# Optimization experiments

Measured on AMD Instinct MI355X. Metric: run time of the kernel, lower is better.

The kernel has to match this reference:

```python
import jax, jax.numpy as jnp
import numpy as np

N_COUNTIES = 3144
P = 2
N_MOB = 6
N_COV = 10
T = 156
NNZ = 31440


def setup_inputs() -> dict:
    key = jax.random.key(0)
    ks = jax.random.split(key, 13)
    C = jax.random.uniform(ks[0], (T, N_COUNTIES), dtype=jnp.float32)
    D = jax.random.uniform(ks[1], (T, N_COUNTIES), dtype=jnp.float32)
    M = jax.random.uniform(ks[2], (N_MOB, T, N_COUNTIES), dtype=jnp.float32)
    cov = jax.random.normal(ks[3], (N_COV, N_COUNTIES), dtype=jnp.float32)
    B_nonzero = jax.random.normal(ks[4], (NNZ,), dtype=jnp.float32)
    A_nonzero = jax.random.normal(ks[5], (NNZ,), dtype=jnp.float32)
    H_nonzero = jax.random.normal(ks[6], (NNZ,), dtype=jnp.float32)
    mu = jax.random.normal(ks[7], (N_MOB, P), dtype=jnp.float32)
    nu = jax.random.normal(ks[8], (N_MOB, P), dtype=jnp.float32)
    upsilon = jax.random.normal(ks[9], (N_COV,), dtype=jnp.float32)
    zeta = jax.random.normal(ks[10], (N_COV,), dtype=jnp.float32)
    rows = jax.random.randint(ks[11], (NNZ,), 0, N_COUNTIES)
    cols = jax.random.randint(ks[12], (NNZ,), 0, N_COUNTIES)
    return dict(C=C, D=D, M=M, cov=cov, B_nonzero=B_nonzero, A_nonzero=A_nonzero,
                H_nonzero=H_nonzero, mu=mu, nu=nu, upsilon=upsilon, zeta=zeta,
                rows=rows, cols=cols)


def reference(C, D, M, cov, B_nonzero, A_nonzero, H_nonzero, mu, nu, upsilon, zeta, rows, cols):
    n = C.shape[1]
    p = mu.shape[1]
    Tp = C.shape[0] - p  # number of predicted steps (t = p .. T-1)

    # Dense scatter-built weight matrices (duplicates summed, matching
    # torch.sparse .to_dense()). The torch code reuses the SAME nonzero
    # vector for every lag tau, so B[tau] == B for all tau.
    B = jnp.zeros((n, n), C.dtype).at[rows, cols].add(B_nonzero)
    A = jnp.zeros((n, n), C.dtype).at[rows, cols].add(A_nonzero)
    H = jnp.zeros((n, n), C.dtype).at[rows, cols].add(H_nonzero)

    # Lagged windows: Cl[tau, i] = C[i + tau] == C[t - p + tau] for t = p + i.
    Cl = jnp.stack([C[tau:tau + Tp] for tau in range(p)], 0)  # [p, Tp, n]
    Dl = jnp.stack([D[tau:tau + Tp] for tau in range(p)], 0)  # [p, Tp, n]
    Ml = jnp.stack([M[:, tau:tau + Tp, :] for tau in range(p)], 1)  # [n_mob, p, Tp, n]

    # Since B[tau] are identical across lags, sum over p folds into one GEMM.
    c2c = jnp.einsum('ptn,nm->tm', Cl, B)  # [Tp, n]
    c2d = jnp.einsum('ptn,nm->tm', Cl, H)
    d2d = jnp.einsum('ptn,nm->tm', Dl, A)

    mob_c = jnp.einsum('kptn,kp->tn', Ml, mu)
    mob_d = jnp.einsum('kptn,kp->tn', Ml, nu)

    C_hat = c2c + mob_c + upsilon @ cov  # [Tp, n] (+ broadcast [n])
    D_hat = c2d + d2d + mob_d + zeta @ cov
    return C_hat, D_hat
```

## Files before the change

kernel.cpp:

```cpp
#include <hip/hip_runtime.h>


#define SCAN_TH 1024

__global__ void hist_and_transposeCD(const int* __restrict__ cols, int* __restrict__ counts,
                                     int NNZ,
                                     const float* __restrict__ C, const float* __restrict__ D,
                                     float* __restrict__ Ct, float* __restrict__ Dt,
                                     int T, int NC, int histBlocks, int cTiles, int tTiles) {
    if ((int)blockIdx.x < histBlocks) {
        int k = blockIdx.x * blockDim.x + threadIdx.x;
        if (k < NNZ) atomicAdd(&counts[cols[k]], 1);
        return;
    }
    __shared__ float tile[64][65];
    int bid = blockIdx.x - histBlocks;
    int z  = bid / (cTiles * tTiles);
    int r  = bid - z * cTiles * tTiles;
    int ct = r / tTiles;
    int tt = r - ct * tTiles;
    const float* src = z ? D : C;
    float* dst = z ? Dt : Ct;
    int lx = threadIdx.x & 63, ly = threadIdx.x >> 6;
    int c0 = ct * 64, t0 = tt * 64;
    for (int rr = ly; rr < 64; rr += 4) {
        int t = t0 + rr, c = c0 + lx;
        if (t < T && c < NC) tile[rr][lx] = src[(size_t)t * NC + c];
    }
    __syncthreads();
    for (int rr = ly; rr < 64; rr += 4) {
        int c = c0 + rr, t = t0 + lx;
        if (c < NC && t < T) dst[(size_t)c * T + t] = tile[lx][rr];
    }
}

__global__ __launch_bounds__(SCAN_TH)
void csr_scan(const int* __restrict__ counts, int* __restrict__ offsets,
              int* __restrict__ cursor, int NC) {
    __shared__ int ssum[SCAN_TH];
    int t = threadIdx.x;
    int chunk = (NC + SCAN_TH - 1) / SCAN_TH;
    int beg = t * chunk, end = min(beg + chunk, NC);
    int local = 0;
    for (int j = beg; j < end; ++j) local += counts[j];
    ssum[t] = local;
    __syncthreads();
    for (int off = 1; off < SCAN_TH; off <<= 1) {
        int v = (t >= off) ? ssum[t - off] : 0;
        __syncthreads();
        ssum[t] += v;
        __syncthreads();
    }
    int run = ssum[t] - local;
    for (int j = beg; j < end; ++j) {
        offsets[j] = run;
        cursor[j]  = run;
        run += counts[j];
    }
    if (t == SCAN_TH - 1) offsets[NC] = ssum[SCAN_TH - 1];
}

__global__ void csr_fill(const int* __restrict__ rows, const int* __restrict__ cols,
                         const float* __restrict__ Bnz, const float* __restrict__ Anz,
                         const float* __restrict__ Hnz,
                         int* __restrict__ cursor, float4* __restrict__ edges, int NNZ) {
    int k = blockIdx.x * blockDim.x + threadIdx.x;
    if (k >= NNZ) return;
    int s = cols[k];
    int pos = atomicAdd(&cursor[s], 1);
    edges[pos] = make_float4(__int_as_float(rows[k]), Bnz[k], Anz[k], Hnz[k]);
}

__global__ void sparse_wave(const float* __restrict__ Ct, const float* __restrict__ Dt,
                            const int* __restrict__ offsets, const float4* __restrict__ edges,
                            float* __restrict__ wsS0, float* __restrict__ wsS1,
                            int T, int TPn, int nChunks, int nWaves) {
    int gtid = blockIdx.x * blockDim.x + threadIdx.x;
    int wid = gtid >> 6, lane = threadIdx.x & 63;
    if (wid >= nWaves) return;
    int c = wid / nChunks;
    int chunk = wid - c * nChunks;
    int i = chunk * 64 + lane;
    bool valid = i < TPn;
    int isafe = valid ? i : 0;
    float a0 = 0.f, a1 = 0.f;
    int e0 = offsets[c], e1 = offsets[c + 1];
    for (int e = e0; e < e1; ++e) {
        float4 E = edges[e];
        int g = __float_as_int(E.x);
        const float* cr = Ct + (size_t)g * T;
        const float* dr = Dt + (size_t)g * T;
        float cs = cr[isafe] + cr[isafe + 1];
        float ds = dr[isafe] + dr[isafe + 1];
        a0 += cs * E.y;
        a1 += cs * E.w + ds * E.z;
    }
    if (valid) {
        wsS0[(size_t)c * TPn + i] = a0;
        wsS1[(size_t)c * TPn + i] = a1;
    }
}

#define FTI 32
#define FTC 32
__global__ void final_fuse(const float* __restrict__ wsS0, const float* __restrict__ wsS1,
                           const float* __restrict__ M,
                           const float* __restrict__ cov,
                           const float* __restrict__ mu,
                           const float* __restrict__ nu,
                           const float* __restrict__ ups, const float* __restrict__ zet,
                           float* __restrict__ out0, float* __restrict__ out1,
                           int T, int NC, int NMOB, int NCOV, int TPn, int cTiles) {
    __shared__ float s0[FTI][FTC + 1], s1[FTI][FTC + 1];
    int bi = blockIdx.x / cTiles;
    int bc = blockIdx.x - bi * cTiles;
    int i0 = bi * FTI, c0 = bc * FTC;
    int tid = threadIdx.x;

    {
        int li = tid & 31;
        int lc0 = tid >> 5;
        int i = i0 + li;
        for (int cc = lc0; cc < FTC; cc += 8) {
            int c = c0 + cc;
            float v0 = 0.f, v1 = 0.f;
            if (c < NC && i < TPn) {
                v0 = wsS0[(size_t)c * TPn + i];
                v1 = wsS1[(size_t)c * TPn + i];
            }
            s0[li][cc] = v0;
            s1[li][cc] = v1;
        }
    }
    __syncthreads();

    int lc = tid & 31;
    int ri = tid >> 5;
    int c = c0 + lc;
    if (c >= NC) return;

    float cv0 = 0.f, cv1 = 0.f;
    for (int j = 0; j < NCOV; ++j) {
        float cv = cov[(size_t)j * NC + c];
        cv0 += cv * ups[j];
        cv1 += cv * zet[j];
    }
    for (int ii = ri; ii < FTI; ii += 8) {
        int i = i0 + ii;
        if (i >= TPn) break;
        float a0 = s0[ii][lc] + cv0;
        float a1 = s1[ii][lc] + cv1;
        for (int k = 0; k < NMOB; ++k) {
            const float* mb = M + (size_t)k * T * NC;
            float m0 = mb[(size_t)i * NC + c];
            float m1 = mb[(size_t)(i + 1) * NC + c];
            a0 += m0 * mu[k * 2] + m1 * mu[k * 2 + 1];
            a1 += m0 * nu[k * 2] + m1 * nu[k * 2 + 1];
        }
        out0[(size_t)i * NC + c] = a0;
        out1[(size_t)i * NC + c] = a1;
    }
}

__global__ void fused_generic(const float* __restrict__ C, const float* __restrict__ D,
                              const float* __restrict__ M, const float* __restrict__ cov,
                              const float* __restrict__ mu, const float* __restrict__ nu,
                              const float* __restrict__ ups, const float* __restrict__ zet,
                              const int* __restrict__ offsets, const float4* __restrict__ edges,
                              float* __restrict__ out0, float* __restrict__ out1,
                              int T, int NC, int NMOB, int NCOV, int P, int TPn) {
    int idx = blockIdx.x * blockDim.x + threadIdx.x;
    if (idx >= TPn * NC) return;
    int i = idx / NC;
    int c = idx - i * NC;
    float acc0 = 0.f, acc1 = 0.f;
    for (int k = 0; k < NMOB; ++k)
        for (int tau = 0; tau < P; ++tau) {
            float m = M[((size_t)k * T + i + tau) * NC + c];
            acc0 += m * mu[k * P + tau];
            acc1 += m * nu[k * P + tau];
        }
    for (int j = 0; j < NCOV; ++j) {
        float cv = cov[(size_t)j * NC + c];
        acc0 += cv * ups[j];
        acc1 += cv * zet[j];
    }
    int e0 = offsets[c], e1 = offsets[c + 1];
    for (int e = e0; e < e1; ++e) {
        float4 E = edges[e];
        int g = __float_as_int(E.x);
        float cs = 0.f, ds = 0.f;
        for (int tau = 0; tau < P; ++tau) {
            cs += C[(size_t)(i + tau) * NC + g];
            ds += D[(size_t)(i + tau) * NC + g];
        }
        acc0 += cs * E.y;
        acc1 += cs * E.w + ds * E.z;
    }
    out0[idx] = acc0;
    out1[idx] = acc1;
}

extern "C" void kernel_launch(void* const* d_in, const int* in_sizes, int n_in,
                              void* d_out, int out_size, void* d_ws, size_t ws_size,
                              hipStream_t stream) {
    const float* C    = (const float*)d_in[0];
    const float* D    = (const float*)d_in[1];
    const float* M    = (const float*)d_in[2];
    const float* cov  = (const float*)d_in[3];
    const float* Bnz  = (const float*)d_in[4];
    const float* Anz  = (const float*)d_in[5];
    const float* Hnz  = (const float*)d_in[6];
    const float* mu   = (const float*)d_in[7];
    const float* nu   = (const float*)d_in[8];
    const float* ups  = (const float*)d_in[9];
    const float* zet  = (const float*)d_in[10];
    const int*  rows  = (const int*)d_in[11];
    const int*  cols  = (const int*)d_in[12];

    int NCOV = in_sizes[9];
    int NC   = in_sizes[3] / NCOV;
    int T    = in_sizes[0] / NC;
    int NMOB = in_sizes[2] / in_sizes[0];
    int P    = in_sizes[7] / NMOB;
    int NNZ  = in_sizes[11];
    int TPn  = T - P;

    float* out0 = (float*)d_out;
    float* out1 = out0 + (size_t)TPn * NC;

    float4* edges   = (float4*)d_ws;
    int*    offsets = (int*)(edges + NNZ);
    int*    counts  = offsets + (NC + 1);
    int*    cursor  = counts + NC;
    float*  Ct      = (float*)(cursor + NC);
    float*  Dt      = Ct + (size_t)NC * T;
    float*  wsS0    = Dt + (size_t)NC * T;
    float*  wsS1    = wsS0 + (size_t)NC * TPn;
    size_t  need    = (size_t)((char*)(wsS1 + (size_t)NC * TPn) - (char*)d_ws);

    const int BS = 256;
    hipMemsetAsync(counts, 0, (size_t)NC * sizeof(int), stream);

    if (P == 2 && ws_size >= need) {
        int histBlocks = (NNZ + BS - 1) / BS;
        int cT64 = (NC + 63) / 64, tT64 = (T + 63) / 64;
        hist_and_transposeCD<<<histBlocks + 2 * cT64 * tT64, BS, 0, stream>>>(
            cols, counts, NNZ, C, D, Ct, Dt, T, NC, histBlocks, cT64, tT64);

        csr_scan<<<1, SCAN_TH, 0, stream>>>(counts, offsets, cursor, NC);
        csr_fill<<<(NNZ + BS - 1) / BS, BS, 0, stream>>>(
            rows, cols, Bnz, Anz, Hnz, cursor, edges, NNZ);

        int nChunks = (TPn + 63) / 64;
        int nWaves  = NC * nChunks;
        sparse_wave<<<(nWaves * 64 + BS - 1) / BS, BS, 0, stream>>>(
            Ct, Dt, offsets, edges, wsS0, wsS1, T, TPn, nChunks, nWaves);

        int iTiles = (TPn + FTI - 1) / FTI;
        int cTiles = (NC + FTC - 1) / FTC;
        final_fuse<<<iTiles * cTiles, BS, 0, stream>>>(
            wsS0, wsS1, M, cov, mu, nu, ups, zet,
            out0, out1, T, NC, NMOB, NCOV, TPn, cTiles);
    } else {
        csr_hist_only:;
        hist_and_transposeCD<<<(NNZ + BS - 1) / BS, BS, 0, stream>>>(
            cols, counts, NNZ, C, D, (float*)d_ws, (float*)d_ws, T, NC,
            (NNZ + BS - 1) / BS, 0, 0);
        csr_scan<<<1, SCAN_TH, 0, stream>>>(counts, offsets, cursor, NC);
        csr_fill<<<(NNZ + BS - 1) / BS, BS, 0, stream>>>(
            rows, cols, Bnz, Anz, Hnz, cursor, edges, NNZ);
        int n = TPn * NC;
        fused_generic<<<(n + BS - 1) / BS, BS, 0, stream>>>(
            C, D, M, cov, mu, nu, ups, zet, offsets, edges,
            out0, out1, T, NC, NMOB, NCOV, P, TPn);
    }
}
```

Before: 141.8 us.

## Replace CSR build and two-stage sparse pass with per-tile edge filtering megakernel

```diff
diff --git a/kernel.cpp b/kernel.cpp
--- a/kernel.cpp
+++ b/kernel.cpp
@@ -1,24 +1,21 @@
 #include <hip/hip_runtime.h>
 
 
+#define BS     256
+#define CTILE  32
+#define ITILE  32
+#define ECAP   3072
 #define SCAN_TH 1024
 
-__global__ void hist_and_transposeCD(const int* __restrict__ cols, int* __restrict__ counts,
-                                     int NNZ,
-                                     const float* __restrict__ C, const float* __restrict__ D,
-                                     float* __restrict__ Ct, float* __restrict__ Dt,
-                                     int T, int NC, int histBlocks, int cTiles, int tTiles) {
-    if ((int)blockIdx.x < histBlocks) {
-        int k = blockIdx.x * blockDim.x + threadIdx.x;
-        if (k < NNZ) atomicAdd(&counts[cols[k]], 1);
-        return;
-    }
+__global__ void transposeCD(const float* __restrict__ C, const float* __restrict__ D,
+                            float* __restrict__ Ct, float* __restrict__ Dt,
+                            int T, int NC, int cT, int tT) {
     __shared__ float tile[64][65];
-    int bid = blockIdx.x - histBlocks;
-    int z  = bid / (cTiles * tTiles);
-    int r  = bid - z * cTiles * tTiles;
-    int ct = r / tTiles;
-    int tt = r - ct * tTiles;
+    int bid = blockIdx.x;
+    int z  = bid / (cT * tT);
+    int r  = bid - z * cT * tT;
+    int ct = r / tT;
+    int tt = r - ct * tT;
     const float* src = z ? D : C;
     float* dst = z ? Dt : Ct;
     int lx = threadIdx.x & 63, ly = threadIdx.x >> 6;
@@ -34,6 +31,127 @@
     }
 }
 
+__global__ __launch_bounds__(BS)
+void mega(const float* __restrict__ Ct,
+          const float* __restrict__ Dt,
+          const float* __restrict__ M,
+          const float* __restrict__ cov,
+          const float* __restrict__ mu,
+          const float* __restrict__ nu,
+          const float* __restrict__ ups,
+          const float* __restrict__ zet,
+          const int*  __restrict__ rows,
+          const int*  __restrict__ cols,
+          const float* __restrict__ Bnz,
+          const float* __restrict__ Anz,
+          const float* __restrict__ Hnz,
+          float* __restrict__ out0, float* __restrict__ out1,
+          int T, int NC, int NMOB, int NCOV, int NNZ, int TPn, int cTiles) {
+    __shared__ int   s_edge[ECAP];
+    __shared__ float s_a0[CTILE][ITILE + 1];
+    __shared__ float s_a1[CTILE][ITILE + 1];
+    __shared__ int   s_scan[BS];
+
+    int bi = blockIdx.x / cTiles;
+    int bc = blockIdx.x - bi * cTiles;
+    int i0 = bi * ITILE, c0 = bc * CTILE;
+    int tid = threadIdx.x;
+    int cmax = NC - c0; if (cmax > CTILE) cmax = CTILE;
+
+    for (int x = tid; x < CTILE * (ITILE + 1); x += BS) {
+        ((float*)s_a0)[x] = 0.f;
+        ((float*)s_a1)[x] = 0.f;
+    }
+
+    int cnt = 0;
+    for (int k = tid; k < NNZ; k += BS) {
+        int cl = cols[k] - c0;
+        if ((unsigned)cl < (unsigned)cmax) cnt++;
+    }
+    s_scan[tid] = cnt;
+    __syncthreads();
+    for (int off = 1; off < BS; off <<= 1) {
+        int v = (tid >= off) ? s_scan[tid - off] : 0;
+        __syncthreads();
+        s_scan[tid] += v;
+        __syncthreads();
+    }
+    int total = s_scan[BS - 1];
+    int wpos = s_scan[tid] - cnt;
+    if (total <= ECAP) {
+        for (int k = tid; k < NNZ; k += BS) {
+            int cl = cols[k] - c0;
+            if ((unsigned)cl < (unsigned)cmax) s_edge[wpos++] = (k << 5) | cl;
+        }
+    }
+    __syncthreads();
+
+    int li  = tid & 31;
+    int grp = tid >> 5;
+    int iA  = i0 + li;
+    int isafe = (iA < TPn) ? iA : (TPn - 1);
+    if (total <= ECAP) {
+        for (int e = grp; e < total; e += 8) {
+            int pk = s_edge[e];
+            int k = pk >> 5, cl = pk & 31;
+            int g = rows[k];
+            float Bv = Bnz[k], Av = Anz[k], Hv = Hnz[k];
+            const float* cr = Ct + (size_t)g * T;
+            const float* dr = Dt + (size_t)g * T;
+            float cs = cr[isafe] + cr[isafe + 1];
+            float ds = dr[isafe] + dr[isafe + 1];
+            atomicAdd(&s_a0[cl][li], cs * Bv);
+            atomicAdd(&s_a1[cl][li], cs * Hv + ds * Av);
+        }
+    } else {
+        for (int k = grp; k < NNZ; k += 8) {
+            int cl = cols[k] - c0;
+            if ((unsigned)cl < (unsigned)cmax) {
+                int g = rows[k];
+                float Bv = Bnz[k], Av = Anz[k], Hv = Hnz[k];
+                const float* cr = Ct + (size_t)g * T;
+                const float* dr = Dt + (size_t)g * T;
+                float cs = cr[isafe] + cr[isafe + 1];
+                float ds = dr[isafe] + dr[isafe + 1];
+                atomicAdd(&s_a0[cl][li], cs * Bv);
+                atomicAdd(&s_a1[cl][li], cs * Hv + ds * Av);
+            }
+        }
+    }
+    __syncthreads();
+
+    int lc = tid & 31;
+    int ri = tid >> 5;
+    int c = c0 + lc;
+    if (c >= NC) return;
+
+    float cv0 = 0.f, cv1 = 0.f;
+    for (int j = 0; j < NCOV; ++j) {
+        float cv = cov[(size_t)j * NC + c];
+        cv0 += cv * ups[j];
+        cv1 += cv * zet[j];
+    }
+    for (int ii = ri; ii < ITILE; ii += 8) {
+        int io = i0 + ii;
+        if (io >= TPn) break;
+        float a0 = s_a0[lc][ii] + cv0;
+        float a1 = s_a1[lc][ii] + cv1;
+        for (int k = 0; k < NMOB; ++k) {
+            const float* mb = M + (size_t)k * T * NC;
+            float m0 = mb[(size_t)io * NC + c];
+            float m1 = mb[(size_t)(io + 1) * NC + c];
+            a0 += m0 * mu[k * 2] + m1 * mu[k * 2 + 1];
+            a1 += m0 * nu[k * 2] + m1 * nu[k * 2 + 1];
+        }
+        out0[(size_t)io * NC + c] = a0;
+        out1[(size_t)io * NC + c] = a1;
+    }
+}
+
+__global__ void csr_hist(const int* __restrict__ cols, int* __restrict__ counts, int NNZ) {
+    int k = blockIdx.x * blockDim.x + threadIdx.x;
+    if (k < NNZ) atomicAdd(&counts[cols[k]], 1);
+}
 __global__ __launch_bounds__(SCAN_TH)
 void csr_scan(const int* __restrict__ counts, int* __restrict__ offsets,
               int* __restrict__ cursor, int NC) {
@@ -59,7 +177,6 @@
     }
     if (t == SCAN_TH - 1) offsets[NC] = ssum[SCAN_TH - 1];
 }
-
 __global__ void csr_fill(const int* __restrict__ rows, const int* __restrict__ cols,
                          const float* __restrict__ Bnz, const float* __restrict__ Anz,
                          const float* __restrict__ Hnz,
@@ -70,98 +187,6 @@
     int pos = atomicAdd(&cursor[s], 1);
     edges[pos] = make_float4(__int_as_float(rows[k]), Bnz[k], Anz[k], Hnz[k]);
 }
-
-__global__ void sparse_wave(const float* __restrict__ Ct, const float* __restrict__ Dt,
-                            const int* __restrict__ offsets, const float4* __restrict__ edges,
-                            float* __restrict__ wsS0, float* __restrict__ wsS1,
-                            int T, int TPn, int nChunks, int nWaves) {
-    int gtid = blockIdx.x * blockDim.x + threadIdx.x;
-    int wid = gtid >> 6, lane = threadIdx.x & 63;
-    if (wid >= nWaves) return;
-    int c = wid / nChunks;
-    int chunk = wid - c * nChunks;
-    int i = chunk * 64 + lane;
-    bool valid = i < TPn;
-    int isafe = valid ? i : 0;
-    float a0 = 0.f, a1 = 0.f;
-    int e0 = offsets[c], e1 = offsets[c + 1];
-    for (int e = e0; e < e1; ++e) {
-        float4 E = edges[e];
-        int g = __float_as_int(E.x);
-        const float* cr = Ct + (size_t)g * T;
-        const float* dr = Dt + (size_t)g * T;
-        float cs = cr[isafe] + cr[isafe + 1];
-        float ds = dr[isafe] + dr[isafe + 1];
-        a0 += cs * E.y;
-        a1 += cs * E.w + ds * E.z;
-    }
-    if (valid) {
-        wsS0[(size_t)c * TPn + i] = a0;
-        wsS1[(size_t)c * TPn + i] = a1;
-    }
-}
-
-#define FTI 32
-#define FTC 32
-__global__ void final_fuse(const float* __restrict__ wsS0, const float* __restrict__ wsS1,
-                           const float* __restrict__ M,
-                           const float* __restrict__ cov,
-                           const float* __restrict__ mu,
-                           const float* __restrict__ nu,
-                           const float* __restrict__ ups, const float* __restrict__ zet,
-                           float* __restrict__ out0, float* __restrict__ out1,
-                           int T, int NC, int NMOB, int NCOV, int TPn, int cTiles) {
-    __shared__ float s0[FTI][FTC + 1], s1[FTI][FTC + 1];
-    int bi = blockIdx.x / cTiles;
-    int bc = blockIdx.x - bi * cTiles;
-    int i0 = bi * FTI, c0 = bc * FTC;
-    int tid = threadIdx.x;
-
-    {
-        int li = tid & 31;
-        int lc0 = tid >> 5;
-        int i = i0 + li;
-        for (int cc = lc0; cc < FTC; cc += 8) {
-            int c = c0 + cc;
-            float v0 = 0.f, v1 = 0.f;
-            if (c < NC && i < TPn) {
-                v0 = wsS0[(size_t)c * TPn + i];
-                v1 = wsS1[(size_t)c * TPn + i];
-            }
-            s0[li][cc] = v0;
-            s1[li][cc] = v1;
-        }
-    }
-    __syncthreads();
-
-    int lc = tid & 31;
-    int ri = tid >> 5;
-    int c = c0 + lc;
-    if (c >= NC) return;
-
-    float cv0 = 0.f, cv1 = 0.f;
-    for (int j = 0; j < NCOV; ++j) {
-        float cv = cov[(size_t)j * NC + c];
-        cv0 += cv * ups[j];
-        cv1 += cv * zet[j];
-    }
-    for (int ii = ri; ii < FTI; ii += 8) {
-        int i = i0 + ii;
-        if (i >= TPn) break;
-        float a0 = s0[ii][lc] + cv0;
-        float a1 = s1[ii][lc] + cv1;
-        for (int k = 0; k < NMOB; ++k) {
-            const float* mb = M + (size_t)k * T * NC;
-            float m0 = mb[(size_t)i * NC + c];
-            float m1 = mb[(size_t)(i + 1) * NC + c];
-            a0 += m0 * mu[k * 2] + m1 * mu[k * 2 + 1];
-            a1 += m0 * nu[k * 2] + m1 * nu[k * 2 + 1];
-        }
-        out0[(size_t)i * NC + c] = a0;
-        out1[(size_t)i * NC + c] = a1;
-    }
-}
-
 __global__ void fused_generic(const float* __restrict__ C, const float* __restrict__ D,
                               const float* __restrict__ M, const float* __restrict__ cov,
                               const float* __restrict__ mu, const float* __restrict__ nu,
@@ -235,38 +260,20 @@
     int*    cursor  = counts + NC;
     float*  Ct      = (float*)(cursor + NC);
     float*  Dt      = Ct + (size_t)NC * T;
-    float*  wsS0    = Dt + (size_t)NC * T;
-    float*  wsS1    = wsS0 + (size_t)NC * TPn;
-    size_t  need    = (size_t)((char*)(wsS1 + (size_t)NC * TPn) - (char*)d_ws);
-
-    const int BS = 256;
-    hipMemsetAsync(counts, 0, (size_t)NC * sizeof(int), stream);
-
-    if (P == 2 && ws_size >= need) {
-        int histBlocks = (NNZ + BS - 1) / BS;
-        int cT64 = (NC + 63) / 64, tT64 = (T + 63) / 64;
-        hist_and_transposeCD<<<histBlocks + 2 * cT64 * tT64, BS, 0, stream>>>(
-            cols, counts, NNZ, C, D, Ct, Dt, T, NC, histBlocks, cT64, tT64);
-
-        csr_scan<<<1, SCAN_TH, 0, stream>>>(counts, offsets, cursor, NC);
-        csr_fill<<<(NNZ + BS - 1) / BS, BS, 0, stream>>>(
-            rows, cols, Bnz, Anz, Hnz, cursor, edges, NNZ);
-
-        int nChunks = (TPn + 63) / 64;
-        int nWaves  = NC * nChunks;
-        sparse_wave<<<(nWaves * 64 + BS - 1) / BS, BS, 0, stream>>>(
-            Ct, Dt, offsets, edges, wsS0, wsS1, T, TPn, nChunks, nWaves);
-
-        int iTiles = (TPn + FTI - 1) / FTI;
-        int cTiles = (NC + FTC - 1) / FTC;
-        final_fuse<<<iTiles * cTiles, BS, 0, stream>>>(
-            wsS0, wsS1, M, cov, mu, nu, ups, zet,
-            out0, out1, T, NC, NMOB, NCOV, TPn, cTiles);
+    size_t  need    = (size_t)((char*)(Dt + (size_t)NC * T) - (char*)d_ws);
+
+    if (P == 2 && ws_size >= need && NNZ < (1 << 26)) {
+        int cT = (NC + 63) / 64, tT = (T + 63) / 64;
+        transposeCD<<<2 * cT * tT, BS, 0, stream>>>(C, D, Ct, Dt, T, NC, cT, tT);
+
+        int iTiles = (TPn + ITILE - 1) / ITILE;
+        int cTiles = (NC + CTILE - 1) / CTILE;
+        mega<<<iTiles * cTiles, BS, 0, stream>>>(
+            Ct, Dt, M, cov, mu, nu, ups, zet, rows, cols, Bnz, Anz, Hnz,
+            out0, out1, T, NC, NMOB, NCOV, NNZ, TPn, cTiles);
     } else {
-        csr_hist_only:;
-        hist_and_transposeCD<<<(NNZ + BS - 1) / BS, BS, 0, stream>>>(
-            cols, counts, NNZ, C, D, (float*)d_ws, (float*)d_ws, T, NC,
-            (NNZ + BS - 1) / BS, 0, 0);
+        hipMemsetAsync(counts, 0, (size_t)NC * sizeof(int), stream);
+        csr_hist<<<(NNZ + BS - 1) / BS, BS, 0, stream>>>(cols, counts, NNZ);
         csr_scan<<<1, SCAN_TH, 0, stream>>>(counts, offsets, cursor, NC);
         csr_fill<<<(NNZ + BS - 1) / BS, BS, 0, stream>>>(
             rows, cols, Bnz, Anz, Hnz, cursor, edges, NNZ);
```

New measurement: 201.7 us. 42.2% more time.

## Fuse transpose, edge bucketing, sparse gather and epilogue into one cooperative kernel

Applied to the files above, without the earlier changes.

```diff
diff --git a/kernel.cpp b/kernel.cpp
--- a/kernel.cpp
+++ b/kernel.cpp
@@ -1,13 +1,163 @@
 #include <hip/hip_runtime.h>
-
-
+#include <hip/hip_cooperative_groups.h>
+namespace cg = cooperative_groups;
+
+
+#define BS      256
+#define ECAP    64
+#define SPILLC  4096
 #define SCAN_TH 1024
+
+__global__ __launch_bounds__(BS)
+void coop_all(const float* __restrict__ C, const float* __restrict__ D,
+              const float* __restrict__ M, const float* __restrict__ cov,
+              const float* __restrict__ mu, const float* __restrict__ nu,
+              const float* __restrict__ ups, const float* __restrict__ zet,
+              const int* __restrict__ rows, const int* __restrict__ cols,
+              const float* __restrict__ Bnz, const float* __restrict__ Anz,
+              const float* __restrict__ Hnz,
+              float* __restrict__ Ct, float* __restrict__ Dt,
+              float4* __restrict__ edges, int* __restrict__ cnt,
+              int* __restrict__ spill_cnt, int* __restrict__ spill,
+              float* __restrict__ out0, float* __restrict__ out1,
+              int T, int NC, int NMOB, int NCOV, int NNZ, int TPn,
+              int cT64, int tT64, int cTiles, int nTiles) {
+    cg::grid_group grid = cg::this_grid();
+    __shared__ float tile[64][65];
+    __shared__ float s_a0[32][33];
+    __shared__ float s_a1[32][33];
+
+    int bid = blockIdx.x, tid = threadIdx.x;
+    int nB = gridDim.x;
+
+    int tTiles = cT64 * tT64;
+    for (int w = bid; w < 2 * tTiles; w += nB) {
+        int z = w / tTiles;
+        int r = w - z * tTiles;
+        int ct = r / tT64, tt = r - ct * tT64;
+        const float* src = z ? D : C;
+        float* dst = z ? Dt : Ct;
+        int lx = tid & 63, ly = tid >> 6;
+        int c0 = ct * 64, t0 = tt * 64;
+        for (int rr = ly; rr < 64; rr += 4) {
+            int t = t0 + rr, c = c0 + lx;
+            if (t < T && c < NC) tile[rr][lx] = src[(size_t)t * NC + c];
+        }
+        __syncthreads();
+        for (int rr = ly; rr < 64; rr += 4) {
+            int c = c0 + rr, t = t0 + lx;
+            if (c < NC && t < T) dst[(size_t)c * T + t] = tile[lx][rr];
+        }
+        __syncthreads();
+    }
+    for (int j = bid * BS + tid; j < NC; j += nB * BS) cnt[j] = 0;
+    if (bid == 0 && tid == 0) *spill_cnt = 0;
+    grid.sync();
+
+    for (int k = bid * BS + tid; k < NNZ; k += nB * BS) {
+        int c = cols[k];
+        int j = atomicAdd(&cnt[c], 1);
+        if (j < ECAP)
+            edges[(size_t)c * ECAP + j] =
+                make_float4(__int_as_float(rows[k]), Bnz[k], Anz[k], Hnz[k]);
+        else {
+            int sp = atomicAdd(spill_cnt, 1);
+            if (sp < SPILLC) spill[sp] = k;
+        }
+    }
+    grid.sync();
+
+    for (int t = bid; t < nTiles; t += nB) {
+        int bi = t / cTiles, bc = t - bi * cTiles;
+        int i0 = bi * 32, c0 = bc * 32;
+        int cmax = NC - c0; if (cmax > 32) cmax = 32;
+
+        int grp = tid >> 5, li = tid & 31;
+        int iA = i0 + li;
+        int isafe = (iA < TPn) ? iA : (TPn - 1);
+        for (int cl = grp; cl < 32; cl += 8) {
+            float a0 = 0.f, a1 = 0.f;
+            if (cl < cmax) {
+                int c = c0 + cl;
+                int n = cnt[c]; if (n > ECAP) n = ECAP;
+                const float4* eb = edges + (size_t)c * ECAP;
+                for (int j = 0; j < n; ++j) {
+                    float4 E = eb[j];
+                    int g = __float_as_int(E.x);
+                    const float* cr = Ct + (size_t)g * T;
+                    const float* dr = Dt + (size_t)g * T;
+                    float cs = cr[isafe] + cr[isafe + 1];
+                    float ds = dr[isafe] + dr[isafe + 1];
+                    a0 += cs * E.y;
+                    a1 += cs * E.w + ds * E.z;
+                }
+            }
+            s_a0[cl][li] = a0;
+            s_a1[cl][li] = a1;
+        }
+        __syncthreads();
+
+        int lc = tid & 31, ri = tid >> 5;
+        int c = c0 + lc;
+        if (c < NC) {
+            float cv0 = 0.f, cv1 = 0.f;
+            for (int j = 0; j < NCOV; ++j) {
+                float cv = cov[(size_t)j * NC + c];
+                cv0 += cv * ups[j];
+                cv1 += cv * zet[j];
+            }
+            for (int ii = ri; ii < 32; ii += 8) {
+                int io = i0 + ii;
+                if (io < TPn) {
+                    float a0 = s_a0[lc][ii] + cv0;
+                    float a1 = s_a1[lc][ii] + cv1;
+                    for (int k = 0; k < NMOB; ++k) {
+                        const float* mb = M + (size_t)k * T * NC;
+                        float m0 = mb[(size_t)io * NC + c];
+                        float m1 = mb[(size_t)(io + 1) * NC + c];
+                        a0 += m0 * mu[k * 2] + m1 * mu[k * 2 + 1];
+                        a1 += m0 * nu[k * 2] + m1 * nu[k * 2 + 1];
+                    }
+                    out0[(size_t)io * NC + c] = a0;
+                    out1[(size_t)io * NC + c] = a1;
+                }
+            }
+        }
+        __syncthreads();
+    }
+
+    int nsp = *spill_cnt;
+    if (nsp > 0) {
+        if (nsp > SPILLC) nsp = SPILLC;
+        for (int t = bid; t < nTiles; t += nB) {
+            int bi = t / cTiles, bc = t - bi * cTiles;
+            int i0 = bi * 32, c0 = bc * 32;
+            int cmax = NC - c0; if (cmax > 32) cmax = 32;
+            if (tid < 32) {
+                int io = i0 + tid;
+                if (io < TPn) {
+                    for (int s = 0; s < nsp; ++s) {
+                        int k = spill[s];
+                        int c = cols[k];
+                        if (c >= c0 && c < c0 + cmax) {
+                            int g = rows[k];
+                            float cs = Ct[(size_t)g * T + io] + Ct[(size_t)g * T + io + 1];
+                            float ds = Dt[(size_t)g * T + io] + Dt[(size_t)g * T + io + 1];
+                            atomicAdd(&out0[(size_t)io * NC + c], cs * Bnz[k]);
+                            atomicAdd(&out1[(size_t)io * NC + c], cs * Hnz[k] + ds * Anz[k]);
+                        }
+                    }
+                }
+            }
+        }
+    }
+}
 
 __global__ void hist_and_transposeCD(const int* __restrict__ cols, int* __restrict__ counts,
                                      int NNZ,
                                      const float* __restrict__ C, const float* __restrict__ D,
                                      float* __restrict__ Ct, float* __restrict__ Dt,
-                                     int T, int NC, int histBlocks, int cTiles, int tTiles) {
+                                     int T, int NC, int histBlocks, int cT, int tT) {
     if ((int)blockIdx.x < histBlocks) {
         int k = blockIdx.x * blockDim.x + threadIdx.x;
         if (k < NNZ) atomicAdd(&counts[cols[k]], 1);
@@ -15,10 +165,9 @@
     }
     __shared__ float tile[64][65];
     int bid = blockIdx.x - histBlocks;
-    int z  = bid / (cTiles * tTiles);
-    int r  = bid - z * cTiles * tTiles;
-    int ct = r / tTiles;
-    int tt = r - ct * tTiles;
+    int z = bid / (cT * tT);
+    int r = bid - z * cT * tT;
+    int ct = r / tT, tt = r - ct * tT;
     const float* src = z ? D : C;
     float* dst = z ? Dt : Ct;
     int lx = threadIdx.x & 63, ly = threadIdx.x >> 6;
@@ -69,97 +218,6 @@
     int s = cols[k];
     int pos = atomicAdd(&cursor[s], 1);
     edges[pos] = make_float4(__int_as_float(rows[k]), Bnz[k], Anz[k], Hnz[k]);
-}
-
-__global__ void sparse_wave(const float* __restrict__ Ct, const float* __restrict__ Dt,
-                            const int* __restrict__ offsets, const float4* __restrict__ edges,
-                            float* __restrict__ wsS0, float* __restrict__ wsS1,
-                            int T, int TPn, int nChunks, int nWaves) {
-    int gtid = blockIdx.x * blockDim.x + threadIdx.x;
-    int wid = gtid >> 6, lane = threadIdx.x & 63;
-    if (wid >= nWaves) return;
-    int c = wid / nChunks;
-    int chunk = wid - c * nChunks;
-    int i = chunk * 64 + lane;
-    bool valid = i < TPn;
-    int isafe = valid ? i : 0;
-    float a0 = 0.f, a1 = 0.f;
-    int e0 = offsets[c], e1 = offsets[c + 1];
-    for (int e = e0; e < e1; ++e) {
-        float4 E = edges[e];
-        int g = __float_as_int(E.x);
-        const float* cr = Ct + (size_t)g * T;
-        const float* dr = Dt + (size_t)g * T;
-        float cs = cr[isafe] + cr[isafe + 1];
-        float ds = dr[isafe] + dr[isafe + 1];
-        a0 += cs * E.y;
-        a1 += cs * E.w + ds * E.z;
-    }
-    if (valid) {
-        wsS0[(size_t)c * TPn + i] = a0;
-        wsS1[(size_t)c * TPn + i] = a1;
-    }
-}
-
-#define FTI 32
-#define FTC 32
-__global__ void final_fuse(const float* __restrict__ wsS0, const float* __restrict__ wsS1,
-                           const float* __restrict__ M,
-                           const float* __restrict__ cov,
-                           const float* __restrict__ mu,
-                           const float* __restrict__ nu,
-                           const float* __restrict__ ups, const float* __restrict__ zet,
-                           float* __restrict__ out0, float* __restrict__ out1,
-                           int T, int NC, int NMOB, int NCOV, int TPn, int cTiles) {
-    __shared__ float s0[FTI][FTC + 1], s1[FTI][FTC + 1];
-    int bi = blockIdx.x / cTiles;
-    int bc = blockIdx.x - bi * cTiles;
-    int i0 = bi * FTI, c0 = bc * FTC;
-    int tid = threadIdx.x;
-
-    {
-        int li = tid & 31;
-        int lc0 = tid >> 5;
-        int i = i0 + li;
-        for (int cc = lc0; cc < FTC; cc += 8) {
-            int c = c0 + cc;
-            float v0 = 0.f, v1 = 0.f;
-            if (c < NC && i < TPn) {
-                v0 = wsS0[(size_t)c * TPn + i];
-                v1 = wsS1[(size_t)c * TPn + i];
-            }
-            s0[li][cc] = v0;
-            s1[li][cc] = v1;
-        }
-    }
-    __syncthreads();
-
-    int lc = tid & 31;
-    int ri = tid >> 5;
-    int c = c0 + lc;
-    if (c >= NC) return;
-
-    float cv0 = 0.f, cv1 = 0.f;
-    for (int j = 0; j < NCOV; ++j) {
-        float cv = cov[(size_t)j * NC + c];
-        cv0 += cv * ups[j];
-        cv1 += cv * zet[j];
-    }
-    for (int ii = ri; ii < FTI; ii += 8) {
-        int i = i0 + ii;
-        if (i >= TPn) break;
-        float a0 = s0[ii][lc] + cv0;
-        float a1 = s1[ii][lc] + cv1;
-        for (int k = 0; k < NMOB; ++k) {
-            const float* mb = M + (size_t)k * T * NC;
-            float m0 = mb[(size_t)i * NC + c];
-            float m1 = mb[(size_t)(i + 1) * NC + c];
-            a0 += m0 * mu[k * 2] + m1 * mu[k * 2 + 1];
-            a1 += m0 * nu[k * 2] + m1 * nu[k * 2 + 1];
-        }
-        out0[(size_t)i * NC + c] = a0;
-        out1[(size_t)i * NC + c] = a1;
-    }
 }
 
 __global__ void fused_generic(const float* __restrict__ C, const float* __restrict__ D,
@@ -230,49 +288,51 @@
     float* out1 = out0 + (size_t)TPn * NC;
 
     float4* edges   = (float4*)d_ws;
-    int*    offsets = (int*)(edges + NNZ);
-    int*    counts  = offsets + (NC + 1);
-    int*    cursor  = counts + NC;
-    float*  Ct      = (float*)(cursor + NC);
+    float*  Ct      = (float*)(edges + (size_t)NC * ECAP);
     float*  Dt      = Ct + (size_t)NC * T;
-    float*  wsS0    = Dt + (size_t)NC * T;
-    float*  wsS1    = wsS0 + (size_t)NC * TPn;
-    size_t  need    = (size_t)((char*)(wsS1 + (size_t)NC * TPn) - (char*)d_ws);
-
-    const int BS = 256;
-    hipMemsetAsync(counts, 0, (size_t)NC * sizeof(int), stream);
-
-    if (P == 2 && ws_size >= need) {
-        int histBlocks = (NNZ + BS - 1) / BS;
-        int cT64 = (NC + 63) / 64, tT64 = (T + 63) / 64;
-        hist_and_transposeCD<<<histBlocks + 2 * cT64 * tT64, BS, 0, stream>>>(
-            cols, counts, NNZ, C, D, Ct, Dt, T, NC, histBlocks, cT64, tT64);
-
-        csr_scan<<<1, SCAN_TH, 0, stream>>>(counts, offsets, cursor, NC);
+    int*    cnt     = (int*)(Dt + (size_t)NC * T);
+    int*    spillc  = cnt + NC;
+    int*    spill   = spillc + 1;
+    size_t  need    = (size_t)((char*)(spill + SPILLC) - (char*)d_ws);
+
+    int cT64 = (NC + 63) / 64, tT64 = (T + 63) / 64;
+    int cTiles = (NC + 31) / 32;
+    int iTiles = (TPn + 31) / 32;
+    int nTiles = iTiles * cTiles;
+
+    bool coop_ok = false;
+    if (P == 2 && ws_size >= need && nTiles <= 512) {
+        void* args[] = {
+            (void*)&C, (void*)&D, (void*)&M, (void*)&cov,
+            (void*)&mu, (void*)&nu, (void*)&ups, (void*)&zet,
+            (void*)&rows, (void*)&cols, (void*)&Bnz, (void*)&Anz, (void*)&Hnz,
+            (void*)&Ct, (void*)&Dt, (void*)&edges, (void*)&cnt,
+            (void*)&spillc, (void*)&spill, (void*)&out0, (void*)&out1,
+            (void*)&T, (void*)&NC, (void*)&NMOB, (void*)&NCOV, (void*)&NNZ,
+            (void*)&TPn, (void*)&cT64, (void*)&tT64, (void*)&cTiles, (void*)&nTiles
+        };
+        hipError_t err = hipLaunchCooperativeKernel(
+            (const void*)coop_all, dim3(nTiles), dim3(BS), args, 0, stream);
+        coop_ok = (err == hipSuccess);
+    }
+
+    if (!coop_ok) {
+        float4* fedges   = (float4*)d_ws;
+        int*    foffsets = (int*)(fedges + NNZ);
+        int*    fcounts  = foffsets + (NC + 1);
+        int*    fcursor  = fcounts + NC;
+        float*  fCt      = (float*)(fcursor + NC);
+        float*  fDt      = fCt + (size_t)NC * T;
+        (void)fDt;
+        hipMemsetAsync(fcounts, 0, (size_t)NC * sizeof(int), stream);
+        hist_and_transposeCD<<<(NNZ + BS - 1) / BS, BS, 0, stream>>>(
+            cols, fcounts, NNZ, C, D, fCt, fCt, T, NC, (NNZ + BS - 1) / BS, 0, 0);
+        csr_scan<<<1, SCAN_TH, 0, stream>>>(fcounts, foffsets, fcursor, NC);
         csr_fill<<<(NNZ + BS - 1) / BS, BS, 0, stream>>>(
-            rows, cols, Bnz, Anz, Hnz, cursor, edges, NNZ);
-
-        int nChunks = (TPn + 63) / 64;
-        int nWaves  = NC * nChunks;
-        sparse_wave<<<(nWaves * 64 + BS - 1) / BS, BS, 0, stream>>>(
-            Ct, Dt, offsets, edges, wsS0, wsS1, T, TPn, nChunks, nWaves);
-
-        int iTiles = (TPn + FTI - 1) / FTI;
-        int cTiles = (NC + FTC - 1) / FTC;
-        final_fuse<<<iTiles * cTiles, BS, 0, stream>>>(
-            wsS0, wsS1, M, cov, mu, nu, ups, zet,
-            out0, out1, T, NC, NMOB, NCOV, TPn, cTiles);
-    } else {
-        csr_hist_only:;
-        hist_and_transposeCD<<<(NNZ + BS - 1) / BS, BS, 0, stream>>>(
-            cols, counts, NNZ, C, D, (float*)d_ws, (float*)d_ws, T, NC,
-            (NNZ + BS - 1) / BS, 0, 0);
-        csr_scan<<<1, SCAN_TH, 0, stream>>>(counts, offsets, cursor, NC);
-        csr_fill<<<(NNZ + BS - 1) / BS, BS, 0, stream>>>(
-            rows, cols, Bnz, Anz, Hnz, cursor, edges, NNZ);
+            rows, cols, Bnz, Anz, Hnz, fcursor, fedges, NNZ);
         int n = TPn * NC;
         fused_generic<<<(n + BS - 1) / BS, BS, 0, stream>>>(
-            C, D, M, cov, mu, nu, ups, zet, offsets, edges,
+            C, D, M, cov, mu, nu, ups, zet, foffsets, fedges,
             out0, out1, T, NC, NMOB, NCOV, P, TPn);
     }
 }
```

Result: slower. 267.5 us (+88.7%).

## Replace CSR scan/fill with fixed-capacity per-column edge buckets and spill path

Applied to the files above, without the earlier changes.

```diff
diff --git a/kernel.cpp b/kernel.cpp
--- a/kernel.cpp
+++ b/kernel.cpp
@@ -1,24 +1,40 @@
 #include <hip/hip_runtime.h>
 
 
+#define BS      256
+#define ECAP    64
+#define SPILLC  4096
 #define SCAN_TH 1024
 
-__global__ void hist_and_transposeCD(const int* __restrict__ cols, int* __restrict__ counts,
-                                     int NNZ,
-                                     const float* __restrict__ C, const float* __restrict__ D,
-                                     float* __restrict__ Ct, float* __restrict__ Dt,
-                                     int T, int NC, int histBlocks, int cTiles, int tTiles) {
-    if ((int)blockIdx.x < histBlocks) {
-        int k = blockIdx.x * blockDim.x + threadIdx.x;
-        if (k < NNZ) atomicAdd(&counts[cols[k]], 1);
+__global__ void prep(const int* __restrict__ rows, const int* __restrict__ cols,
+                     const float* __restrict__ Bnz, const float* __restrict__ Anz,
+                     const float* __restrict__ Hnz,
+                     const float* __restrict__ C, const float* __restrict__ D,
+                     float* __restrict__ Ct, float* __restrict__ Dt,
+                     float4* __restrict__ edges, int* __restrict__ cnt,
+                     int* __restrict__ spill_cnt, int* __restrict__ spill,
+                     int T, int NC, int NNZ, int fillBlocks, int cT64, int tT64) {
+    if ((int)blockIdx.x < fillBlocks) {
+        int k = blockIdx.x * BS + threadIdx.x;
+        if (k < NNZ) {
+            int c = cols[k];
+            int j = atomicAdd(&cnt[c], 1);
+            if (j < ECAP)
+                edges[(size_t)c * ECAP + j] =
+                    make_float4(__int_as_float(rows[k]), Bnz[k], Anz[k], Hnz[k]);
+            else {
+                int sp = atomicAdd(spill_cnt, 1);
+                if (sp < SPILLC) spill[sp] = k;
+            }
+        }
         return;
     }
     __shared__ float tile[64][65];
-    int bid = blockIdx.x - histBlocks;
-    int z  = bid / (cTiles * tTiles);
-    int r  = bid - z * cTiles * tTiles;
-    int ct = r / tTiles;
-    int tt = r - ct * tTiles;
+    int bid = blockIdx.x - fillBlocks;
+    int tTiles = cT64 * tT64;
+    int z = bid / tTiles;
+    int r = bid - z * tTiles;
+    int ct = r / tT64, tt = r - ct * tT64;
     const float* src = z ? D : C;
     float* dst = z ? Dt : Ct;
     int lx = threadIdx.x & 63, ly = threadIdx.x >> 6;
@@ -34,6 +50,130 @@
     }
 }
 
+__global__ void sparse_wave(const float* __restrict__ Ct, const float* __restrict__ Dt,
+                            const int* __restrict__ cnt, const float4* __restrict__ edges,
+                            float* __restrict__ wsS0, float* __restrict__ wsS1,
+                            int T, int TPn, int nChunks, int nWaves) {
+    int gtid = blockIdx.x * blockDim.x + threadIdx.x;
+    int wid = gtid >> 6, lane = threadIdx.x & 63;
+    if (wid >= nWaves) return;
+    int c = wid / nChunks;
+    int chunk = wid - c * nChunks;
+    int i = chunk * 64 + lane;
+    bool valid = i < TPn;
+    int isafe = valid ? i : 0;
+    float a0 = 0.f, a1 = 0.f;
+    int n = cnt[c]; if (n > ECAP) n = ECAP;
+    const float4* eb = edges + (size_t)c * ECAP;
+    for (int j = 0; j < n; ++j) {
+        float4 E = eb[j];
+        int g = __float_as_int(E.x);
+        const float* cr = Ct + (size_t)g * T;
+        const float* dr = Dt + (size_t)g * T;
+        float cs = cr[isafe] + cr[isafe + 1];
+        float ds = dr[isafe] + dr[isafe + 1];
+        a0 += cs * E.y;
+        a1 += cs * E.w + ds * E.z;
+    }
+    if (valid) {
+        wsS0[(size_t)c * TPn + i] = a0;
+        wsS1[(size_t)c * TPn + i] = a1;
+    }
+}
+
+#define FTI 32
+#define FTC 32
+__global__ void final_fuse(const float* __restrict__ wsS0, const float* __restrict__ wsS1,
+                           const float* __restrict__ M,
+                           const float* __restrict__ cov,
+                           const float* __restrict__ mu,
+                           const float* __restrict__ nu,
+                           const float* __restrict__ ups, const float* __restrict__ zet,
+                           const float* __restrict__ Ct, const float* __restrict__ Dt,
+                           const int* __restrict__ rows, const int* __restrict__ cols,
+                           const float* __restrict__ Bnz, const float* __restrict__ Anz,
+                           const float* __restrict__ Hnz,
+                           const int* __restrict__ spill_cnt, const int* __restrict__ spill,
+                           float* __restrict__ out0, float* __restrict__ out1,
+                           int T, int NC, int NMOB, int NCOV, int TPn, int cTiles) {
+    __shared__ float s0[FTI][FTC + 1], s1[FTI][FTC + 1];
+    int bi = blockIdx.x / cTiles;
+    int bc = blockIdx.x - bi * cTiles;
+    int i0 = bi * FTI, c0 = bc * FTC;
+    int tid = threadIdx.x;
+
+    {
+        int li = tid & 31;
+        int lc0 = tid >> 5;
+        int i = i0 + li;
+        for (int cc = lc0; cc < FTC; cc += 8) {
+            int c = c0 + cc;
+            float v0 = 0.f, v1 = 0.f;
+            if (c < NC && i < TPn) {
+                v0 = wsS0[(size_t)c * TPn + i];
+                v1 = wsS1[(size_t)c * TPn + i];
+            }
+            s0[li][cc] = v0;
+            s1[li][cc] = v1;
+        }
+    }
+    __syncthreads();
+
+    int lc = tid & 31;
+    int ri = tid >> 5;
+    int c = c0 + lc;
+    if (c < NC) {
+        float cv0 = 0.f, cv1 = 0.f;
+        for (int j = 0; j < NCOV; ++j) {
+            float cv = cov[(size_t)j * NC + c];
+            cv0 += cv * ups[j];
+            cv1 += cv * zet[j];
+        }
+        for (int ii = ri; ii < FTI; ii += 8) {
+            int i = i0 + ii;
+            if (i >= TPn) break;
+            float a0 = s0[ii][lc] + cv0;
+            float a1 = s1[ii][lc] + cv1;
+            for (int k = 0; k < NMOB; ++k) {
+                const float* mb = M + (size_t)k * T * NC;
+                float m0 = mb[(size_t)i * NC + c];
+                float m1 = mb[(size_t)(i + 1) * NC + c];
+                a0 += m0 * mu[k * 2] + m1 * mu[k * 2 + 1];
+                a1 += m0 * nu[k * 2] + m1 * nu[k * 2 + 1];
+            }
+            out0[(size_t)i * NC + c] = a0;
+            out1[(size_t)i * NC + c] = a1;
+        }
+    }
+
+    int nsp = *spill_cnt;
+    if (nsp > 0) {
+        __syncthreads();
+        if (nsp > SPILLC) nsp = SPILLC;
+        int cmax = NC - c0; if (cmax > FTC) cmax = FTC;
+        if (tid < FTI) {
+            int io = i0 + tid;
+            if (io < TPn) {
+                for (int s = 0; s < nsp; ++s) {
+                    int k = spill[s];
+                    int cc = cols[k];
+                    if (cc >= c0 && cc < c0 + cmax) {
+                        int g = rows[k];
+                        float cs = Ct[(size_t)g * T + io] + Ct[(size_t)g * T + io + 1];
+                        float ds = Dt[(size_t)g * T + io] + Dt[(size_t)g * T + io + 1];
+                        atomicAdd(&out0[(size_t)io * NC + cc], cs * Bnz[k]);
+                        atomicAdd(&out1[(size_t)io * NC + cc], cs * Hnz[k] + ds * Anz[k]);
+                    }
+                }
+            }
+        }
+    }
+}
+
+__global__ void csr_hist(const int* __restrict__ cols, int* __restrict__ counts, int NNZ) {
+    int k = blockIdx.x * blockDim.x + threadIdx.x;
+    if (k < NNZ) atomicAdd(&counts[cols[k]], 1);
+}
 __global__ __launch_bounds__(SCAN_TH)
 void csr_scan(const int* __restrict__ counts, int* __restrict__ offsets,
               int* __restrict__ cursor, int NC) {
@@ -59,7 +199,6 @@
     }
     if (t == SCAN_TH - 1) offsets[NC] = ssum[SCAN_TH - 1];
 }
-
 __global__ void csr_fill(const int* __restrict__ rows, const int* __restrict__ cols,
                          const float* __restrict__ Bnz, const float* __restrict__ Anz,
                          const float* __restrict__ Hnz,
@@ -70,98 +209,6 @@
     int pos = atomicAdd(&cursor[s], 1);
     edges[pos] = make_float4(__int_as_float(rows[k]), Bnz[k], Anz[k], Hnz[k]);
 }
-
-__global__ void sparse_wave(const float* __restrict__ Ct, const float* __restrict__ Dt,
-                            const int* __restrict__ offsets, const float4* __restrict__ edges,
-                            float* __restrict__ wsS0, float* __restrict__ wsS1,
-                            int T, int TPn, int nChunks, int nWaves) {
-    int gtid = blockIdx.x * blockDim.x + threadIdx.x;
-    int wid = gtid >> 6, lane = threadIdx.x & 63;
-    if (wid >= nWaves) return;
-    int c = wid / nChunks;
-    int chunk = wid - c * nChunks;
-    int i = chunk * 64 + lane;
-    bool valid = i < TPn;
-    int isafe = valid ? i : 0;
-    float a0 = 0.f, a1 = 0.f;
-    int e0 = offsets[c], e1 = offsets[c + 1];
-    for (int e = e0; e < e1; ++e) {
-        float4 E = edges[e];
-        int g = __float_as_int(E.x);
-        const float* cr = Ct + (size_t)g * T;
-        const float* dr = Dt + (size_t)g * T;
-        float cs = cr[isafe] + cr[isafe + 1];
-        float ds = dr[isafe] + dr[isafe + 1];
-        a0 += cs * E.y;
-        a1 += cs * E.w + ds * E.z;
-    }
-    if (valid) {
-        wsS0[(size_t)c * TPn + i] = a0;
-        wsS1[(size_t)c * TPn + i] = a1;
-    }
-}
-
-#define FTI 32
-#define FTC 32
-__global__ void final_fuse(const float* __restrict__ wsS0, const float* __restrict__ wsS1,
-                           const float* __restrict__ M,
-                           const float* __restrict__ cov,
-                           const float* __restrict__ mu,
-                           const float* __restrict__ nu,
-                           const float* __restrict__ ups, const float* __restrict__ zet,
-                           float* __restrict__ out0, float* __restrict__ out1,
-                           int T, int NC, int NMOB, int NCOV, int TPn, int cTiles) {
-    __shared__ float s0[FTI][FTC + 1], s1[FTI][FTC + 1];
-    int bi = blockIdx.x / cTiles;
-    int bc = blockIdx.x - bi * cTiles;
-    int i0 = bi * FTI, c0 = bc * FTC;
-    int tid = threadIdx.x;
-
-    {
-        int li = tid & 31;
-        int lc0 = tid >> 5;
-        int i = i0 + li;
-        for (int cc = lc0; cc < FTC; cc += 8) {
-            int c = c0 + cc;
-            float v0 = 0.f, v1 = 0.f;
-            if (c < NC && i < TPn) {
-                v0 = wsS0[(size_t)c * TPn + i];
-                v1 = wsS1[(size_t)c * TPn + i];
-            }
-            s0[li][cc] = v0;
-            s1[li][cc] = v1;
-        }
-    }
-    __syncthreads();
-
-    int lc = tid & 31;
-    int ri = tid >> 5;
-    int c = c0 + lc;
-    if (c >= NC) return;
-
-    float cv0 = 0.f, cv1 = 0.f;
-    for (int j = 0; j < NCOV; ++j) {
-        float cv = cov[(size_t)j * NC + c];
-        cv0 += cv * ups[j];
-        cv1 += cv * zet[j];
-    }
-    for (int ii = ri; ii < FTI; ii += 8) {
-        int i = i0 + ii;
-        if (i >= TPn) break;
-        float a0 = s0[ii][lc] + cv0;
-        float a1 = s1[ii][lc] + cv1;
-        for (int k = 0; k < NMOB; ++k) {
-            const float* mb = M + (size_t)k * T * NC;
-            float m0 = mb[(size_t)i * NC + c];
-            float m1 = mb[(size_t)(i + 1) * NC + c];
-            a0 += m0 * mu[k * 2] + m1 * mu[k * 2 + 1];
-            a1 += m0 * nu[k * 2] + m1 * nu[k * 2 + 1];
-        }
-        out0[(size_t)i * NC + c] = a0;
-        out1[(size_t)i * NC + c] = a1;
-    }
-}
-
 __global__ void fused_generic(const float* __restrict__ C, const float* __restrict__ D,
                               const float* __restrict__ M, const float* __restrict__ cov,
                               const float* __restrict__ mu, const float* __restrict__ nu,
@@ -229,50 +276,49 @@
     float* out0 = (float*)d_out;
     float* out1 = out0 + (size_t)TPn * NC;
 
-    float4* edges   = (float4*)d_ws;
-    int*    offsets = (int*)(edges + NNZ);
-    int*    counts  = offsets + (NC + 1);
-    int*    cursor  = counts + NC;
-    float*  Ct      = (float*)(cursor + NC);
-    float*  Dt      = Ct + (size_t)NC * T;
-    float*  wsS0    = Dt + (size_t)NC * T;
-    float*  wsS1    = wsS0 + (size_t)NC * TPn;
-    size_t  need    = (size_t)((char*)(wsS1 + (size_t)NC * TPn) - (char*)d_ws);
-
-    const int BS = 256;
-    hipMemsetAsync(counts, 0, (size_t)NC * sizeof(int), stream);
+    float4* edges  = (float4*)d_ws;
+    int*    cnt    = (int*)(edges + (size_t)NC * ECAP);
+    int*    spillc = cnt + NC;
+    int*    spill  = spillc + 1;
+    float*  Ct     = (float*)(spill + SPILLC);
+    float*  Dt     = Ct + (size_t)NC * T;
+    float*  wsS0   = Dt + (size_t)NC * T;
+    float*  wsS1   = wsS0 + (size_t)NC * TPn;
+    size_t  need   = (size_t)((char*)(wsS1 + (size_t)NC * TPn) - (char*)d_ws);
 
     if (P == 2 && ws_size >= need) {
-        int histBlocks = (NNZ + BS - 1) / BS;
+        hipMemsetAsync(cnt, 0, (size_t)(NC + 1) * sizeof(int), stream);
+
+        int fillBlocks = (NNZ + BS - 1) / BS;
         int cT64 = (NC + 63) / 64, tT64 = (T + 63) / 64;
-        hist_and_transposeCD<<<histBlocks + 2 * cT64 * tT64, BS, 0, stream>>>(
-            cols, counts, NNZ, C, D, Ct, Dt, T, NC, histBlocks, cT64, tT64);
-
-        csr_scan<<<1, SCAN_TH, 0, stream>>>(counts, offsets, cursor, NC);
-        csr_fill<<<(NNZ + BS - 1) / BS, BS, 0, stream>>>(
-            rows, cols, Bnz, Anz, Hnz, cursor, edges, NNZ);
+        prep<<<fillBlocks + 2 * cT64 * tT64, BS, 0, stream>>>(
+            rows, cols, Bnz, Anz, Hnz, C, D, Ct, Dt,
+            edges, cnt, spillc, spill, T, NC, NNZ, fillBlocks, cT64, tT64);
 
         int nChunks = (TPn + 63) / 64;
         int nWaves  = NC * nChunks;
         sparse_wave<<<(nWaves * 64 + BS - 1) / BS, BS, 0, stream>>>(
-            Ct, Dt, offsets, edges, wsS0, wsS1, T, TPn, nChunks, nWaves);
+            Ct, Dt, cnt, edges, wsS0, wsS1, T, TPn, nChunks, nWaves);
 
         int iTiles = (TPn + FTI - 1) / FTI;
         int cTiles = (NC + FTC - 1) / FTC;
         final_fuse<<<iTiles * cTiles, BS, 0, stream>>>(
-            wsS0, wsS1, M, cov, mu, nu, ups, zet,
+            wsS0, wsS1, M, cov, mu, nu, ups, zet, Ct, Dt,
+            rows, cols, Bnz, Anz, Hnz, spillc, spill,
             out0, out1, T, NC, NMOB, NCOV, TPn, cTiles);
     } else {
-        csr_hist_only:;
-        hist_and_transposeCD<<<(NNZ + BS - 1) / BS, BS, 0, stream>>>(
-            cols, counts, NNZ, C, D, (float*)d_ws, (float*)d_ws, T, NC,
-            (NNZ + BS - 1) / BS, 0, 0);
-        csr_scan<<<1, SCAN_TH, 0, stream>>>(counts, offsets, cursor, NC);
+        float4* fedges   = (float4*)d_ws;
+        int*    foffsets = (int*)(fedges + NNZ);
+        int*    fcounts  = foffsets + (NC + 1);
+        int*    fcursor  = fcounts + NC;
+        hipMemsetAsync(fcounts, 0, (size_t)NC * sizeof(int), stream);
+        csr_hist<<<(NNZ + BS - 1) / BS, BS, 0, stream>>>(cols, fcounts, NNZ);
+        csr_scan<<<1, SCAN_TH, 0, stream>>>(fcounts, foffsets, fcursor, NC);
         csr_fill<<<(NNZ + BS - 1) / BS, BS, 0, stream>>>(
-            rows, cols, Bnz, Anz, Hnz, cursor, edges, NNZ);
+            rows, cols, Bnz, Anz, Hnz, fcursor, fedges, NNZ);
         int n = TPn * NC;
         fused_generic<<<(n + BS - 1) / BS, BS, 0, stream>>>(
-            C, D, M, cov, mu, nu, ups, zet, offsets, edges,
+            C, D, M, cov, mu, nu, ups, zet, foffsets, fedges,
             out0, out1, T, NC, NMOB, NCOV, P, TPn);
     }
 }
```

Measured after the change: 132.8 us. 1.07x faster.
